# Kernel tuning notes

Measured on AMD Instinct MI355X. Metric: run time of the kernel, lower is better.

The kernel has to match this reference:

```python
import jax, jax.numpy as jnp
import numpy as np

N, A, H, W = 8, 3, 336, 336
IMG_W, IMG_H = 1333.0, 800.0
PRE_TOP_K = 2000
POST_NMS_TOP_N = 1000
NMS_THR = 0.7
MIN_SIZE = 0.0
TO_REMOVE = 1.0
XFORM_CLIP = float(np.log(1000.0 / 16.0))
NEG = -1e9


def setup_inputs() -> dict:
    key = jax.random.key(0)
    k1, k2, k3, k4, k5, k6 = jax.random.split(key, 6)
    M = A * H * W
    x1 = jax.random.uniform(k1, (N, M)) * (IMG_W - 1.0)
    y1 = jax.random.uniform(k2, (N, M)) * (IMG_H - 1.0)
    bw = jax.random.uniform(k3, (N, M)) * 256.0 + 4.0
    bh = jax.random.uniform(k4, (N, M)) * 256.0 + 4.0
    anchors = jnp.stack([x1, y1, x1 + bw, y1 + bh], axis=-1).astype(jnp.float32)
    logits = jax.random.normal(k5, (N, A, H, W), dtype=jnp.float32)
    bbox_reg = jax.random.normal(k6, (N, A * 4, H, W), dtype=jnp.float32) * 0.25
    return {"anchors": anchors, "logits": logits, "bbox_reg": bbox_reg}


def _decode(anchors, deltas):
    # anchors, deltas: [..., 4] in xyxy / (dx,dy,dw,dh)
    w = anchors[..., 2] - anchors[..., 0] + TO_REMOVE
    h = anchors[..., 3] - anchors[..., 1] + TO_REMOVE
    cx = anchors[..., 0] + 0.5 * w
    cy = anchors[..., 1] + 0.5 * h
    dx, dy, dw, dh = deltas[..., 0], deltas[..., 1], deltas[..., 2], deltas[..., 3]
    dw = jnp.minimum(dw, XFORM_CLIP)
    dh = jnp.minimum(dh, XFORM_CLIP)
    pcx = dx * w + cx
    pcy = dy * h + cy
    pw = jnp.exp(dw) * w
    ph = jnp.exp(dh) * h
    return jnp.stack([pcx - 0.5 * pw, pcy - 0.5 * ph,
                      pcx + 0.5 * pw - 1.0, pcy + 0.5 * ph - 1.0], axis=-1)


def _nms_single(boxes, scores):
    # boxes: [K,4], scores: [K] (invalid entries already set to NEG)
    areas = (boxes[:, 2] - boxes[:, 0] + TO_REMOVE) * (boxes[:, 3] - boxes[:, 1] + TO_REMOVE)

    def step(live, _):
        j = jnp.argmax(live)
        sj = live[j]
        bj = boxes[j]
        xx1 = jnp.maximum(bj[0], boxes[:, 0])
        yy1 = jnp.maximum(bj[1], boxes[:, 1])
        xx2 = jnp.minimum(bj[2], boxes[:, 2])
        yy2 = jnp.minimum(bj[3], boxes[:, 3])
        inter = jnp.maximum(xx2 - xx1 + TO_REMOVE, 0.0) * jnp.maximum(yy2 - yy1 + TO_REMOVE, 0.0)
        iou = inter / (areas[j] + areas - inter)
        live = jnp.where(iou > NMS_THR, NEG, live)
        live = live.at[j].set(NEG)
        valid = sj > NEG * 0.5
        return live, (jnp.where(valid, bj, 0.0), jnp.where(valid, sj, 0.0))

    _, (sel_boxes, sel_scores) = jax.lax.scan(step, scores, None, length=POST_NMS_TOP_N)
    return sel_boxes, sel_scores


def _forward(anchors, logits, bbox_reg):
    n, a, h, w = logits.shape
    # objectness scores: [N, A*H*W], ordered as (H, W, A) like the torch permute
    scores = jax.nn.sigmoid(jnp.transpose(logits, (0, 2, 3, 1)).reshape(n, -1))
    reg = bbox_reg.reshape(n, a, 4, h, w)
    reg = jnp.transpose(reg, (0, 3, 4, 1, 2)).reshape(n, -1, 4)
    k = min(scores.shape[1], PRE_TOP_K)
    top_scores, idx = jax.lax.top_k(scores, k)  # sorted descending
    reg_k = jnp.take_along_axis(reg, idx[..., None], axis=1)
    anc_k = jnp.take_along_axis(anchors, idx[..., None], axis=1)
    props = _decode(anc_k, reg_k)
    x1 = jnp.clip(props[..., 0], 0.0, IMG_W - 1.0)
    y1 = jnp.clip(props[..., 1], 0.0, IMG_H - 1.0)
    x2 = jnp.clip(props[..., 2], 0.0, IMG_W - 1.0)
    y2 = jnp.clip(props[..., 3], 0.0, IMG_H - 1.0)
    clipped = jnp.stack([x1, y1, x2, y2], axis=-1)
    ws = x2 - x1 + TO_REMOVE
    hs = y2 - y1 + TO_REMOVE
    keep = (ws >= MIN_SIZE) & (hs >= MIN_SIZE)
    sc = jnp.where(keep, top_scores, NEG)
    sel_boxes, sel_scores = jax.vmap(_nms_single)(clipped, sc)
    # [N, POST_NMS_TOP_N, 5] = boxes + score
    return jnp.concatenate([sel_boxes, sel_scores[..., None]], axis=-1)


def reference(anchors, logits, bbox_reg):
    return _forward(anchors, logits, bbox_reg)
```

## Files before the change

### kernel.cpp

```cpp
#include <hip/hip_runtime.h>
#include <stdint.h>

#define N_BATCH 8
#define A_ 3
#define H_ 336
#define W_ 336
#define HW_ (H_*W_)
#define M_ (A_*HW_)
#define K_TOP 2000
#define POST_N 1000
#define NMS_THR_ 0.7f
#define NEG_ (-1e9f)
#define VALID_THR_ (-5e8f)
#define CAND_CAP 4096
#define NBINS 4096
#define BIN_SHIFT 20
#define HBLK 32
#define SEG_ (M_/HBLK)
#define XCLIP 4.135166556742356f

#define NPAD 2048
#define NW 32
#define NCHUNK 32
#define RING 4

typedef unsigned long long u64;

__device__ __forceinline__ unsigned int flip_key(float x) {
    unsigned int u = __float_as_uint(x);
    return (u & 0x80000000u) ? ~u : (u | 0x80000000u);
}
__device__ __forceinline__ float unflip_key(unsigned int k) {
    unsigned int u = (k & 0x80000000u) ? (k & 0x7fffffffu) : ~k;
    return __uint_as_float(u);
}

__device__ __forceinline__ void gload_lds16(const u64* g, u64* l) {
    __builtin_amdgcn_global_load_lds(
        (const __attribute__((address_space(1))) unsigned int*)(const void*)g,
        (__attribute__((address_space(3))) unsigned int*)(void*)l,
        16, 0, 0);
}

__global__ __launch_bounds__(512) void k_hist(const float* __restrict__ logits,
                                              unsigned short* __restrict__ ghist) {
    __shared__ unsigned int h[NBINS];
    int n = blockIdx.y, b = blockIdx.x;
    for (int i = threadIdx.x; i < NBINS; i += 512) h[i] = 0;
    __syncthreads();
    const float4* lp = (const float4*)(logits + (size_t)n * M_ + (size_t)b * SEG_);
    const int nq = SEG_ / 4;
    for (int q = threadIdx.x; q < nq; q += 512) {
        float4 v = lp[q];
        atomicAdd(&h[flip_key(v.x) >> BIN_SHIFT], 1u);
        atomicAdd(&h[flip_key(v.y) >> BIN_SHIFT], 1u);
        atomicAdd(&h[flip_key(v.z) >> BIN_SHIFT], 1u);
        atomicAdd(&h[flip_key(v.w) >> BIN_SHIFT], 1u);
    }
    __syncthreads();
    unsigned short* gp = ghist + ((size_t)n * HBLK + b) * NBINS;
    for (int i = threadIdx.x; i < NBINS; i += 512) gp[i] = (unsigned short)h[i];
}

__global__ __launch_bounds__(256) void k_scan(const unsigned short* __restrict__ ghist,
                                              unsigned int* __restrict__ thresh) {
    int n = blockIdx.x;
    int t = threadIdx.x;
    __shared__ unsigned int binsum[NBINS];
    __shared__ unsigned int part[256];
    __shared__ unsigned int scanb[256];
    const unsigned short* base = ghist + (size_t)n * HBLK * NBINS;
    for (int i = t; i < NBINS; i += 256) {
        unsigned int s = 0;
        #pragma unroll 8
        for (int b = 0; b < HBLK; ++b) s += base[(size_t)b * NBINS + i];
        binsum[i] = s;
    }
    __syncthreads();
    int hi = NBINS - 16 * t;
    int lo = hi - 16;
    unsigned int s = 0;
    for (int b = lo; b < hi; ++b) s += binsum[b];
    part[t] = s;
    scanb[t] = s;
    __syncthreads();
    for (int off = 1; off < 256; off <<= 1) {
        unsigned int v = scanb[t];
        unsigned int addv = (t >= off) ? scanb[t - off] : 0u;
        __syncthreads();
        scanb[t] = v + addv;
        __syncthreads();
    }
    unsigned int incl = scanb[t];
    unsigned int prefix = incl - part[t];
    if (prefix < K_TOP && incl >= K_TOP) {
        unsigned int acc = prefix;
        for (int b = hi - 1; b >= lo; --b) {
            unsigned int c = binsum[b];
            if (acc + c >= K_TOP) {
                thresh[n] = (unsigned int)b;
                break;
            }
            acc += c;
        }
    }
}

__global__ __launch_bounds__(512) void k_compact(const float* __restrict__ logits,
                                                 const unsigned int* __restrict__ thresh,
                                                 unsigned int* __restrict__ cnt,
                                                 u64* __restrict__ cand) {
    __shared__ u64 buf[CAND_CAP];
    __shared__ unsigned int lcnt;
    __shared__ unsigned int gbase;
    int n = blockIdx.y, b = blockIdx.x;
    unsigned int B = thresh[n];
    if (threadIdx.x == 0) lcnt = 0;
    __syncthreads();
    const int qbase = b * SEG_;
    const float4* lp = (const float4*)(logits + (size_t)n * M_ + (size_t)qbase);
    const int nq = SEG_ / 4;
    for (int q = threadIdx.x; q < nq; q += 512) {
        float4 v = lp[q];
        float vv[4] = {v.x, v.y, v.z, v.w};
        #pragma unroll
        for (int e = 0; e < 4; ++e) {
            unsigned int u = flip_key(vv[e]);
            if ((u >> BIN_SHIFT) >= B) {
                int qq = qbase + q * 4 + e;
                int a = qq / HW_;
                int hw = qq - a * HW_;
                unsigned int m = (unsigned int)(hw * A_ + a);
                unsigned int pos = atomicAdd(&lcnt, 1u);
                if (pos < CAND_CAP)
                    buf[pos] = ((u64)u << 32) | (unsigned int)(~m);
            }
        }
    }
    __syncthreads();
    unsigned int L = (lcnt < CAND_CAP) ? lcnt : CAND_CAP;
    if (threadIdx.x == 0) gbase = atomicAdd(&cnt[n], L);
    __syncthreads();
    u64* cp = cand + (size_t)n * CAND_CAP;
    for (unsigned int i = threadIdx.x; i < L; i += 512) {
        unsigned int pos = gbase + i;
        if (pos < CAND_CAP) cp[pos] = buf[i];
    }
}

__global__ __launch_bounds__(512) void k_rank(const u64* __restrict__ cand,
                                              const unsigned int* __restrict__ cnt,
                                              const float* __restrict__ anchors,
                                              const float* __restrict__ breg,
                                              float4* __restrict__ boxes,
                                              float* __restrict__ scores,
                                              float* __restrict__ areas) {
    __shared__ u64 keys[CAND_CAP];
    __shared__ unsigned short psum[512];
    int n = blockIdx.y;
    int bx = blockIdx.x;
    unsigned int Cu = cnt[n];
    int C = (Cu < CAND_CAP) ? (int)Cu : CAND_CAP;
    const u64* cp = cand + (size_t)n * CAND_CAP;
    for (int i = threadIdx.x; i < C; i += 512) keys[i] = cp[i];
    __syncthreads();
    int t = threadIdx.x;
    int ci = bx * 256 + (t & 255);
    int half = t >> 8;
    unsigned int r = 0;
    u64 ki = 0;
    if (ci < C) {
        ki = keys[ci];
        int j = half;
        for (; j + 6 < C; j += 8) {
            r += (keys[j] > ki);
            r += (keys[j + 2] > ki);
            r += (keys[j + 4] > ki);
            r += (keys[j + 6] > ki);
        }
        for (; j < C; j += 2) r += (keys[j] > ki);
    }
    psum[t] = (unsigned short)r;
    __syncthreads();
    if (t < 256 && ci < C) {
        unsigned int rank = (unsigned int)psum[t] + (unsigned int)psum[t + 256];
        if (rank < K_TOP) {
            unsigned int u = (unsigned int)(ki >> 32);
            unsigned int m = ~((unsigned int)ki);
            float logit = unflip_key(u);
            int a = (int)(m % 3u);
            int hw = (int)(m / 3u);
            float4 anc = ((const float4*)anchors)[(size_t)n * M_ + m];
            size_t rb = ((size_t)n * 12 + a * 4) * HW_ + hw;
            float dx = breg[rb];
            float dy = breg[rb + (size_t)HW_];
            float dw = breg[rb + (size_t)2 * HW_];
            float dh = breg[rb + (size_t)3 * HW_];
            float score = 1.0f / (1.0f + expf(-logit));
            float w = anc.z - anc.x + 1.0f;
            float h = anc.w - anc.y + 1.0f;
            float cx = anc.x + 0.5f * w;
            float cy = anc.y + 0.5f * h;
            dw = fminf(dw, XCLIP);
            dh = fminf(dh, XCLIP);
            float pcx = dx * w + cx;
            float pcy = dy * h + cy;
            float pw = expf(dw) * w;
            float ph = expf(dh) * h;
            float x1 = pcx - 0.5f * pw;
            float y1 = pcy - 0.5f * ph;
            float x2 = pcx + 0.5f * pw - 1.0f;
            float y2 = pcy + 0.5f * ph - 1.0f;
            x1 = fminf(fmaxf(x1, 0.0f), 1332.0f);
            y1 = fminf(fmaxf(y1, 0.0f), 799.0f);
            x2 = fminf(fmaxf(x2, 0.0f), 1332.0f);
            y2 = fminf(fmaxf(y2, 0.0f), 799.0f);
            float ww = x2 - x1 + 1.0f;
            float hh = y2 - y1 + 1.0f;
            bool keep = (ww >= 0.0f) && (hh >= 0.0f);
            int g = n * K_TOP + (int)rank;
            boxes[g] = make_float4(x1, y1, x2, y2);
            scores[g] = keep ? score : NEG_;
            areas[g] = ww * hh;
        }
    }
}

#define JT 512
#define RT 64
__global__ __launch_bounds__(256) void k_edges(const float4* __restrict__ boxes,
                                               const float* __restrict__ areas,
                                               u64* __restrict__ adj) {
    __shared__ float4 jb[JT];
    __shared__ float ja[JT];
    int n = blockIdx.z;
    int r0 = blockIdx.y * RT;
    int j0 = blockIdx.x * JT;
    for (int j = threadIdx.x; j < JT; j += 256) {
        int jj = j0 + j;
        if (jj < K_TOP) {
            jb[j] = boxes[(size_t)n * K_TOP + jj];
            ja[j] = areas[(size_t)n * K_TOP + jj];
        } else {
            jb[j] = make_float4(-1e8f, -1e8f, -1e8f, -1e8f);
            ja[j] = 0.0f;
        }
    }
    __syncthreads();
    int i = r0 + (threadIdx.x >> 2);
    if (i >= K_TOP) return;
    float4 bi = boxes[(size_t)n * K_TOP + i];
    float ai = areas[(size_t)n * K_TOP + i];
    #pragma unroll
    for (int rep = 0; rep < 2; ++rep) {
        int wl = (threadIdx.x & 3) + rep * 4;
        u64 bits = 0;
        int base = wl * 64;
        #pragma unroll 8
        for (int b = 0; b < 64; ++b) {
            float4 bj = jb[base + b];
            float xx1 = fmaxf(bi.x, bj.x);
            float yy1 = fmaxf(bi.y, bj.y);
            float xx2 = fminf(bi.z, bj.z);
            float yy2 = fminf(bi.w, bj.w);
            float inter = fmaxf(xx2 - xx1 + 1.0f, 0.0f) * fmaxf(yy2 - yy1 + 1.0f, 0.0f);
            float iou = inter / (ai + ja[base + b] - inter);
            bits |= ((u64)(iou > NMS_THR_)) << b;
        }
        adj[((size_t)n * NPAD + i) * NW + (j0 >> 6) + wl] = bits;
    }
}

__global__ __launch_bounds__(256) void k_resolve(const float4* __restrict__ boxes,
                                                 const float* __restrict__ scores,
                                                 const u64* __restrict__ adj,
                                                 float* __restrict__ out) {
    __shared__ u64 ring[RING][64 * NW];
    __shared__ float sls[NPAD];
    __shared__ unsigned char alive[NPAD];
    __shared__ int ready[RING];
    __shared__ int progress;
    __shared__ unsigned int scanbuf[256];
    int n = blockIdx.x;
    int tid = threadIdx.x;
    int wave = tid >> 6, lane = tid & 63;
    const u64* ab = adj + (size_t)n * NPAD * NW;

    for (int i = tid; i < NPAD; i += 256) {
        sls[i] = (i < K_TOP) ? scores[(size_t)n * K_TOP + i] : NEG_;
        alive[i] = 0;
    }
    if (tid < RING) ready[tid] = 0;
    if (tid == 0) progress = 0;
    __syncthreads();

    if (wave == 0) {
        u64 supreg = 0;
        int survTot = 0;
        for (int c = 0; c < NCHUNK; ++c) {
            int slot = c & (RING - 1);
            while (__hip_atomic_load(&ready[slot], __ATOMIC_ACQUIRE,
                                     __HIP_MEMORY_SCOPE_WORKGROUP) != c + 1)
                __builtin_amdgcn_s_sleep(1);
            int k = lane;
            int gi = c * 64 + k;
            u64 colk = ring[slot][k * NW + c];
            u64 supc = __shfl(supreg, c, 64);
            bool validk = (sls[gi] > VALID_THR_) && !((supc >> k) & 1ull);
            u64 below = (k == 0) ? 0ull : ((1ull << k) - 1ull);
            u64 rel = colk & below;
            bool a = validk;
            u64 am = __ballot(a);
            while (true) {
                bool anew = validk && ((am & rel) == 0ull);
                u64 am2 = __ballot(anew);
                if (am2 == am) { a = anew; break; }
                am = am2;
            }
            alive[gi] = a ? 1 : 0;
            int nal = (int)__popcll(am);
            survTot += nal;
            if (survTot >= POST_N) {
                if (lane == 0)
                    __hip_atomic_store(&progress, NCHUNK, __ATOMIC_RELEASE,
                                       __HIP_MEMORY_SCOPE_WORKGROUP);
                break;
            }
            int w = lane & 31, half = lane >> 5;
            u64 acc = 0;
            u64 m = am & (half ? 0xAAAAAAAAAAAAAAAAull : 0x5555555555555555ull);
            while (m) {
                int k1 = __ffsll((unsigned long long)m) - 1; m &= m - 1;
                int k2 = k1, k3 = k1, k4 = k1;
                if (m) { k2 = __ffsll((unsigned long long)m) - 1; m &= m - 1; }
                if (m) { k3 = __ffsll((unsigned long long)m) - 1; m &= m - 1; }
                if (m) { k4 = __ffsll((unsigned long long)m) - 1; m &= m - 1; }
                u64 r1 = ring[slot][k1 * NW + w];
                u64 r2 = ring[slot][k2 * NW + w];
                u64 r3 = ring[slot][k3 * NW + w];
                u64 r4 = ring[slot][k4 * NW + w];
                acc |= r1 | r2 | r3 | r4;
            }
            acc |= __shfl_down(acc, 32);
            if (lane < 32) supreg |= acc;
            if (lane == 0)
                __hip_atomic_store(&progress, c + 1, __ATOMIC_RELEASE,
                                   __HIP_MEMORY_SCOPE_WORKGROUP);
        }
    } else {
        for (int c = wave - 1; c < NCHUNK; c += 3) {
            int slot = c & (RING - 1);
            int p;
            while ((p = __hip_atomic_load(&progress, __ATOMIC_ACQUIRE,
                                          __HIP_MEMORY_SCOPE_WORKGROUP)) < c - 3)
                __builtin_amdgcn_s_sleep(1);
            if (p >= NCHUNK) break;
            const u64* src = ab + (size_t)c * 64 * NW + lane * 2;
            u64* dst = &ring[slot][0];
            #pragma unroll
            for (int it = 0; it < 16; ++it)
                gload_lds16(src + (size_t)it * 128, dst + it * 128);
            __builtin_amdgcn_s_waitcnt(0);
            if (lane == 0)
                __hip_atomic_store(&ready[slot], c + 1, __ATOMIC_RELEASE,
                                   __HIP_MEMORY_SCOPE_WORKGROUP);
        }
    }
    __syncthreads();

    int i0 = tid * 8;
    unsigned int c2 = 0;
    for (int i = i0; i < i0 + 8; ++i) c2 += alive[i];
    scanbuf[tid] = c2;
    __syncthreads();
    for (int off = 1; off < 256; off <<= 1) {
        unsigned int v = scanbuf[tid];
        unsigned int addv = (tid >= off) ? scanbuf[tid - off] : 0u;
        __syncthreads();
        scanbuf[tid] = v + addv;
        __syncthreads();
    }
    unsigned int r = scanbuf[tid] - c2;
    unsigned int total = scanbuf[255];
    float* op = out + (size_t)n * POST_N * 5;
    const float4* bb = boxes + (size_t)n * K_TOP;
    for (int i = i0; i < i0 + 8; ++i) {
        if (alive[i]) {
            if (r < POST_N) {
                float4 b = bb[i];
                op[r * 5 + 0] = b.x;
                op[r * 5 + 1] = b.y;
                op[r * 5 + 2] = b.z;
                op[r * 5 + 3] = b.w;
                op[r * 5 + 4] = sls[i];
            }
            r++;
        }
    }
    unsigned int S = (total > POST_N) ? POST_N : total;
    for (unsigned int q = S + tid; q < POST_N; q += 256) {
        op[q * 5 + 0] = 0.0f;
        op[q * 5 + 1] = 0.0f;
        op[q * 5 + 2] = 0.0f;
        op[q * 5 + 3] = 0.0f;
        op[q * 5 + 4] = 0.0f;
    }
}

extern "C" void kernel_launch(void* const* d_in, const int* in_sizes, int n_in,
                              void* d_out, int out_size, void* d_ws, size_t ws_size,
                              hipStream_t stream) {
    const float* anchors = (const float*)d_in[0];
    const float* logits  = (const float*)d_in[1];
    const float* breg    = (const float*)d_in[2];
    float* out = (float*)d_out;
    char* ws = (char*)d_ws;

    unsigned int* cnt     = (unsigned int*)(ws);
    unsigned int* thresh  = (unsigned int*)(ws + 64);
    unsigned short* ghist = (unsigned short*)(ws + 128);
    u64* cand             = (u64*)(ws + 2097280);
    u64* adj              = (u64*)(ws + 128);
    float4* boxes         = (float4*)(ws + 4194432);
    float* scores         = (float*)(ws + 4450432);
    float* areas          = (float*)(ws + 4514432);

    hipMemsetAsync(ws, 0, 96, stream);

    k_hist<<<dim3(HBLK, 8), 512, 0, stream>>>(logits, ghist);
    k_scan<<<8, 256, 0, stream>>>(ghist, thresh);
    k_compact<<<dim3(HBLK, 8), 512, 0, stream>>>(logits, thresh, cnt, cand);
    k_rank<<<dim3(16, 8), 512, 0, stream>>>(cand, cnt, anchors, breg, boxes, scores, areas);
    k_edges<<<dim3(NPAD / JT, NPAD / RT, 8), 256, 0, stream>>>(boxes, areas, adj);
    k_resolve<<<8, 256, 0, stream>>>(boxes, scores, adj, out);
}
```

Baseline: 223.2 us.

## Fuse scan into compact, drop memset, finer rank split, skip lower-triangle edge tiles

Removes the separate threshold-scan kernel: every compact block now recomputes the per-image histogram prefix scan itself before filtering. The count reset moves into k_hist, which eliminates the memset. k_rank now uses 4 threads per candidate over 32 blocks and exits early when a block has no candidates, and k_edges skips tiles below the diagonal, since suppression only needs j > i. Together these cut launches and wasted work, but each of the 256 compact blocks now re-reads the whole histogram for its image.

After: 197.7 us. -11.4%, faster.

```diff
diff --git a/kernel.cpp b/kernel.cpp
--- a/kernel.cpp
+++ b/kernel.cpp
@@ -23,6 +23,7 @@
 #define NW 32
 #define NCHUNK 32
 #define RING 4
+#define RBLK 128
 
 typedef unsigned long long u64;
 
@@ -43,9 +44,11 @@
 }
 
 __global__ __launch_bounds__(512) void k_hist(const float* __restrict__ logits,
-                                              unsigned short* __restrict__ ghist) {
+                                              unsigned short* __restrict__ ghist,
+                                              unsigned int* __restrict__ cnt) {
     __shared__ unsigned int h[NBINS];
     int n = blockIdx.y, b = blockIdx.x;
+    if (b == 0 && threadIdx.x == 0) cnt[n] = 0;
     for (int i = threadIdx.x; i < NBINS; i += 512) h[i] = 0;
     __syncthreads();
     const float4* lp = (const float4*)(logits + (size_t)n * M_ + (size_t)b * SEG_);
@@ -62,29 +65,36 @@
     for (int i = threadIdx.x; i < NBINS; i += 512) gp[i] = (unsigned short)h[i];
 }
 
-__global__ __launch_bounds__(256) void k_scan(const unsigned short* __restrict__ ghist,
-                                              unsigned int* __restrict__ thresh) {
-    int n = blockIdx.x;
+__global__ __launch_bounds__(512) void k_compact(const float* __restrict__ logits,
+                                                 const unsigned short* __restrict__ ghist,
+                                                 unsigned int* __restrict__ cnt,
+                                                 u64* __restrict__ cand) {
+    __shared__ unsigned int binsum[NBINS];
+    __shared__ unsigned int part[512];
+    __shared__ unsigned int scanb[512];
+    __shared__ u64 buf[CAND_CAP];
+    __shared__ unsigned int lcnt;
+    __shared__ unsigned int gbase;
+    __shared__ int Bsh;
+    int n = blockIdx.y, b = blockIdx.x;
     int t = threadIdx.x;
-    __shared__ unsigned int binsum[NBINS];
-    __shared__ unsigned int part[256];
-    __shared__ unsigned int scanb[256];
+    if (t == 0) lcnt = 0;
     const unsigned short* base = ghist + (size_t)n * HBLK * NBINS;
-    for (int i = t; i < NBINS; i += 256) {
+    for (int i = t; i < NBINS; i += 512) {
         unsigned int s = 0;
         #pragma unroll 8
-        for (int b = 0; b < HBLK; ++b) s += base[(size_t)b * NBINS + i];
+        for (int sb = 0; sb < HBLK; ++sb) s += base[(size_t)sb * NBINS + i];
         binsum[i] = s;
     }
     __syncthreads();
-    int hi = NBINS - 16 * t;
-    int lo = hi - 16;
+    int hi = NBINS - 8 * t;
+    int lo = hi - 8;
     unsigned int s = 0;
-    for (int b = lo; b < hi; ++b) s += binsum[b];
+    for (int bb = lo; bb < hi; ++bb) s += binsum[bb];
     part[t] = s;
     scanb[t] = s;
     __syncthreads();
-    for (int off = 1; off < 256; off <<= 1) {
+    for (int off = 1; off < 512; off <<= 1) {
         unsigned int v = scanb[t];
         unsigned int addv = (t >= off) ? scanb[t - off] : 0u;
         __syncthreads();
@@ -95,32 +105,18 @@
     unsigned int prefix = incl - part[t];
     if (prefix < K_TOP && incl >= K_TOP) {
         unsigned int acc = prefix;
-        for (int b = hi - 1; b >= lo; --b) {
-            unsigned int c = binsum[b];
-            if (acc + c >= K_TOP) {
-                thresh[n] = (unsigned int)b;
-                break;
-            }
+        for (int bb = hi - 1; bb >= lo; --bb) {
+            unsigned int c = binsum[bb];
+            if (acc + c >= K_TOP) { Bsh = bb; break; }
             acc += c;
         }
     }
-}
-
-__global__ __launch_bounds__(512) void k_compact(const float* __restrict__ logits,
-                                                 const unsigned int* __restrict__ thresh,
-                                                 unsigned int* __restrict__ cnt,
-                                                 u64* __restrict__ cand) {
-    __shared__ u64 buf[CAND_CAP];
-    __shared__ unsigned int lcnt;
-    __shared__ unsigned int gbase;
-    int n = blockIdx.y, b = blockIdx.x;
-    unsigned int B = thresh[n];
-    if (threadIdx.x == 0) lcnt = 0;
-    __syncthreads();
+    __syncthreads();
+    unsigned int B = (unsigned int)Bsh;
     const int qbase = b * SEG_;
     const float4* lp = (const float4*)(logits + (size_t)n * M_ + (size_t)qbase);
     const int nq = SEG_ / 4;
-    for (int q = threadIdx.x; q < nq; q += 512) {
+    for (int q = t; q < nq; q += 512) {
         float4 v = lp[q];
         float vv[4] = {v.x, v.y, v.z, v.w};
         #pragma unroll
@@ -139,10 +135,10 @@
     }
     __syncthreads();
     unsigned int L = (lcnt < CAND_CAP) ? lcnt : CAND_CAP;
-    if (threadIdx.x == 0) gbase = atomicAdd(&cnt[n], L);
+    if (t == 0) gbase = atomicAdd(&cnt[n], L);
     __syncthreads();
     u64* cp = cand + (size_t)n * CAND_CAP;
-    for (unsigned int i = threadIdx.x; i < L; i += 512) {
+    for (unsigned int i = t; i < L; i += 512) {
         unsigned int pos = gbase + i;
         if (pos < CAND_CAP) cp[pos] = buf[i];
     }
@@ -161,29 +157,31 @@
     int bx = blockIdx.x;
     unsigned int Cu = cnt[n];
     int C = (Cu < CAND_CAP) ? (int)Cu : CAND_CAP;
+    if (bx * RBLK >= C) return;
     const u64* cp = cand + (size_t)n * CAND_CAP;
     for (int i = threadIdx.x; i < C; i += 512) keys[i] = cp[i];
     __syncthreads();
     int t = threadIdx.x;
-    int ci = bx * 256 + (t & 255);
-    int half = t >> 8;
+    int tq = t & 3;
+    int cl = t >> 2;
+    int ci = bx * RBLK + cl;
     unsigned int r = 0;
     u64 ki = 0;
     if (ci < C) {
         ki = keys[ci];
-        int j = half;
-        for (; j + 6 < C; j += 8) {
+        int j = tq;
+        for (; j + 12 < C; j += 16) {
             r += (keys[j] > ki);
-            r += (keys[j + 2] > ki);
             r += (keys[j + 4] > ki);
-            r += (keys[j + 6] > ki);
-        }
-        for (; j < C; j += 2) r += (keys[j] > ki);
+            r += (keys[j + 8] > ki);
+            r += (keys[j + 12] > ki);
+        }
+        for (; j < C; j += 4) r += (keys[j] > ki);
     }
     psum[t] = (unsigned short)r;
     __syncthreads();
-    if (t < 256 && ci < C) {
-        unsigned int rank = (unsigned int)psum[t] + (unsigned int)psum[t + 256];
+    if (tq == 0 && ci < C) {
+        unsigned int rank = (unsigned int)psum[t] + psum[t + 1] + psum[t + 2] + psum[t + 3];
         if (rank < K_TOP) {
             unsigned int u = (unsigned int)(ki >> 32);
             unsigned int m = ~((unsigned int)ki);
@@ -231,11 +229,14 @@
 __global__ __launch_bounds__(256) void k_edges(const float4* __restrict__ boxes,
                                                const float* __restrict__ areas,
                                                u64* __restrict__ adj) {
+    int n = blockIdx.z;
+    int by = blockIdx.y;
+    int bx = blockIdx.x;
+    if (by > bx * 8 + 7) return;
     __shared__ float4 jb[JT];
     __shared__ float ja[JT];
-    int n = blockIdx.z;
-    int r0 = blockIdx.y * RT;
-    int j0 = blockIdx.x * JT;
+    int r0 = by * RT;
+    int j0 = bx * JT;
     for (int j = threadIdx.x; j < JT; j += 256) {
         int jj = j0 + j;
         if (jj < K_TOP) {
@@ -417,7 +418,6 @@
     char* ws = (char*)d_ws;
 
     unsigned int* cnt     = (unsigned int*)(ws);
-    unsigned int* thresh  = (unsigned int*)(ws + 64);
     unsigned short* ghist = (unsigned short*)(ws + 128);
     u64* cand             = (u64*)(ws + 2097280);
     u64* adj              = (u64*)(ws + 128);
@@ -425,12 +425,10 @@
     float* scores         = (float*)(ws + 4450432);
     float* areas          = (float*)(ws + 4514432);
 
-    hipMemsetAsync(ws, 0, 96, stream);
-
-    k_hist<<<dim3(HBLK, 8), 512, 0, stream>>>(logits, ghist);
-    k_scan<<<8, 256, 0, stream>>>(ghist, thresh);
-    k_compact<<<dim3(HBLK, 8), 512, 0, stream>>>(logits, thresh, cnt, cand);
-    k_rank<<<dim3(16, 8), 512, 0, stream>>>(cand, cnt, anchors, breg, boxes, scores, areas);
+    k_hist<<<dim3(HBLK, 8), 512, 0, stream>>>(logits, ghist, cnt);
+    k_compact<<<dim3(HBLK, 8), 512, 0, stream>>>(logits, ghist, cnt, cand);
+    k_rank<<<dim3(CAND_CAP / RBLK, 8), 512, 0, stream>>>(cand, cnt, anchors, breg,
+                                                         boxes, scores, areas);
     k_edges<<<dim3(NPAD / JT, NPAD / RT, 8), 256, 0, stream>>>(boxes, areas, adj);
     k_resolve<<<8, 256, 0, stream>>>(boxes, scores, adj, out);
 }
```
